# Kernel tuning notes

Measured on AMD Instinct MI355X. Metric: run time of the kernel, lower is better.

Reference implementation:

```python
import jax, jax.numpy as jnp
import numpy as np

HEADS = 4
DIM_HEAD = 64
SCALE = 8.0
EPS = 1e-5  # fp32 branch of the original LayerNorm


def setup_inputs() -> dict:
    key = jax.random.key(0)
    k1, k2, k3 = jax.random.split(key, 3)
    B, C, F, H, W = 2, 256, 4, 32, 32
    inner = HEADS * DIM_HEAD  # 256
    x = jax.random.normal(k1, (B, C, F, H, W), dtype=jnp.float32)
    gamma = jnp.ones((1, C, 1, 1, 1), dtype=jnp.float32)
    w_qkv = jax.random.normal(k2, (3 * inner, C), dtype=jnp.float32) * 0.05
    w_out = jax.random.normal(k3, (C, inner), dtype=jnp.float32) * 0.05
    return {"x": x, "gamma": gamma, "w_qkv": w_qkv, "w_out": w_out}


def _l2norm(t):
    return t / jnp.sqrt(jnp.sum(t * t, axis=-1, keepdims=True) + 1e-12)


def reference(x, gamma, w_qkv, w_out):
    B, C, F, H, W = x.shape
    N = F * H * W
    inner = HEADS * DIM_HEAD
    residual = x

    # channel LayerNorm (biased variance over dim=1)
    mean = jnp.mean(x, axis=1, keepdims=True)
    var = jnp.mean((x - mean) ** 2, axis=1, keepdims=True)
    xn = (x - mean) / jnp.sqrt(var + EPS) * gamma

    # 1x1x1 conv == channel matmul; flatten spatial dims to sequence
    xn_flat = xn.reshape(B, C, N)                      # [B, C, N]
    qkv = jnp.einsum('oc,bcn->bon', w_qkv, xn_flat)    # [B, 3*inner, N]
    qkv = qkv.reshape(B, 3, HEADS, DIM_HEAD, N)        # chunk then split heads
    qkv = jnp.transpose(qkv, (1, 0, 2, 4, 3))          # [3, B, h, N, d]
    q, k, v = qkv[0], qkv[1], qkv[2]

    q = _l2norm(q)
    k = _l2norm(k)

    sim = jnp.einsum('bhid,bhjd->bhij', q, k) * SCALE  # [B, h, N, N]
    attn = jax.nn.softmax(sim, axis=-1)
    out = jnp.einsum('bhij,bhjd->bhid', attn, v)       # [B, h, N, d]

    # 'b h n d -> b (h d) n' then 1x1x1 out conv
    out = jnp.transpose(out, (0, 1, 3, 2)).reshape(B, inner, N)
    out = jnp.einsum('oi,bin->bon', w_out, out).reshape(B, C, F, H, W)
    return out + residual
```

## Files before the change

### kernel.cpp

```cpp
#include <hip/hip_runtime.h>

#define BATCH 2
#define CCH   256
#define NSEQ  4096
#define NH    4
#define DH    64
#define INNER 256

typedef __attribute__((ext_vector_type(8))) __bf16 bf16x8;
typedef __attribute__((ext_vector_type(4))) float f32x4;
typedef __attribute__((ext_vector_type(8))) unsigned short u16x8;
typedef __attribute__((ext_vector_type(4))) unsigned short u16x4;
typedef __attribute__((ext_vector_type(4))) short s16x4;

#define GLD16(gsrc, ldst)                                                     \
  __builtin_amdgcn_global_load_lds(                                           \
      (const __attribute__((address_space(1))) unsigned int*)(const void*)(gsrc), \
      (__attribute__((address_space(3))) unsigned int*)(void*)(ldst), 16, 0, 0)

static __device__ __forceinline__ unsigned short f2bfr(float f) {
  union { float f; unsigned u; } v; v.f = f;
  return (unsigned short)((v.u + 0x8000u) >> 16);
}
static __device__ __forceinline__ unsigned pack2(float f0, float f1) {
  union { float f; unsigned u; } a, b; a.f = f0; b.f = f1;
  return __builtin_amdgcn_perm(b.u + 0x8000u, a.u + 0x8000u, 0x07060302u);
}
static __device__ __forceinline__ float bf2f(unsigned short u) {
  union { unsigned u; float f; } v; v.u = ((unsigned)u) << 16;
  return v.f;
}
static __device__ __forceinline__ bf16x8 ldb(const unsigned short* p) {
  return *(const bf16x8*)p;
}
static __device__ __forceinline__ f32x4 mm(bf16x8 a, bf16x8 b, f32x4 c) {
  return __builtin_amdgcn_mfma_f32_16x16x32_bf16(a, b, c, 0, 0, 0);
}
static __device__ __forceinline__ f32x4 mm16(s16x4 a, s16x4 b, f32x4 c) {
  return __builtin_amdgcn_mfma_f32_16x16x16bf16_1k(a, b, c, 0, 0, 0);
}

__global__ __launch_bounds__(256) void k_lncvt(const float* __restrict__ x,
                                               const float* __restrict__ gamma,
                                               unsigned short* __restrict__ xn,
                                               const float* __restrict__ wq,
                                               const float* __restrict__ wo,
                                               unsigned short* __restrict__ wqb,
                                               unsigned short* __restrict__ wob) {
  int blk = blockIdx.x;
  if (blk >= 256) {
    int t = (blk - 256) * 256 + threadIdx.x;
    int e = t * 4;
    if (e < 768 * 256) {
      float4 v = *(const float4*)(wq + e);
      u16x4 pk = { f2bfr(v.x), f2bfr(v.y), f2bfr(v.z), f2bfr(v.w) };
      *(u16x4*)(wqb + e) = pk;
    } else {
      int e2 = e - 768 * 256;
      float4 v = *(const float4*)(wo + e2);
      u16x4 pk = { f2bfr(v.x), f2bfr(v.y), f2bfr(v.z), f2bfr(v.w) };
      *(u16x4*)(wob + e2) = pk;
    }
    return;
  }
  int b  = blk >> 7;
  int n0 = (blk & 127) * 32;
  int t  = threadIdx.x;
  int nl = t & 31;
  int cg = t >> 5;
  int n  = n0 + nl;
  const float* xp = x + ((size_t)(b * CCH + cg * 32)) * NSEQ + n;
  float vals[32];
  float s = 0.f, s2 = 0.f;
#pragma unroll
  for (int j = 0; j < 32; j++) {
    float v = xp[(size_t)j * NSEQ];
    vals[j] = v; s += v; s2 += v * v;
  }
  __shared__ float rs[8][32], rs2[8][32];
  rs[cg][nl] = s; rs2[cg][nl] = s2;
  __syncthreads();
  float S = 0.f, S2 = 0.f;
#pragma unroll
  for (int g = 0; g < 8; g++) { S += rs[g][nl]; S2 += rs2[g][nl]; }
  float mean = S * (1.f / 256.f);
  float var  = S2 * (1.f / 256.f) - mean * mean;
  float rstd = rsqrtf(var + 1e-5f);
  unsigned short* dst = xn + ((size_t)b * NSEQ + n) * CCH + cg * 32;
#pragma unroll
  for (int j0 = 0; j0 < 32; j0 += 8) {
    u16x8 pk;
#pragma unroll
    for (int j = 0; j < 8; j++)
      pk[j] = f2bfr((vals[j0 + j] - mean) * rstd * gamma[cg * 32 + j0 + j]);
    *(u16x8*)(dst + j0) = pk;
  }
}

__global__ __launch_bounds__(256) void k_qkv(const unsigned short* __restrict__ wqb,
                                             const unsigned short* __restrict__ xn,
                                             unsigned short* __restrict__ vtb,
                                             unsigned short* __restrict__ qt,
                                             unsigned short* __restrict__ ktb) {
  int n0 = blockIdx.x * 64;
  int oi = blockIdx.y;
  int o0 = oi * 64;
  int b  = blockIdx.z;
  __shared__ unsigned short Al[64 * 128];
  __shared__ unsigned short Bl[64 * 128];
  int t = threadIdx.x;
  int lane = t & 63, w = t >> 6;
  int c = lane & 15, quad = lane >> 4;
  int wm = w >> 1, wn = w & 1;
  f32x4 acc[2][2] = {};
  int lr = lane >> 4;
  int lchk = lane & 15;
  const unsigned short* apg = wqb + (size_t)o0 * CCH;
  const unsigned short* bpg = xn + ((size_t)b * NSEQ + n0) * CCH;
  for (int kt = 0; kt < 2; kt++) {
    if (kt) __syncthreads();
#pragma unroll
    for (int q = 0; q < 4; q++) {
      int r = w * 16 + q * 4 + lr;
      int srcoff = r * CCH + kt * 128 + ((lchk ^ (r & 7)) * 8);
      GLD16(apg + srcoff, Al + (size_t)(w * 16 + q * 4) * 128);
      GLD16(bpg + srcoff, Bl + (size_t)(w * 16 + q * 4) * 128);
    }
    __syncthreads();
#pragma unroll
    for (int ks = 0; ks < 4; ks++) {
      int ra0 = wm * 32 + c, ra1 = ra0 + 16;
      int rb0 = wn * 32 + c, rb1 = rb0 + 16;
      bf16x8 a0 = ldb(&Al[ra0 * 128 + (((ks * 4 + quad) ^ (ra0 & 7)) * 8)]);
      bf16x8 a1 = ldb(&Al[ra1 * 128 + (((ks * 4 + quad) ^ (ra1 & 7)) * 8)]);
      bf16x8 b0 = ldb(&Bl[rb0 * 128 + (((ks * 4 + quad) ^ (rb0 & 7)) * 8)]);
      bf16x8 b1 = ldb(&Bl[rb1 * 128 + (((ks * 4 + quad) ^ (rb1 & 7)) * 8)]);
      acc[0][0] = mm(a0, b0, acc[0][0]);
      acc[0][1] = mm(a0, b1, acc[0][1]);
      acc[1][0] = mm(a1, b0, acc[1][0]);
      acc[1][1] = mm(a1, b1, acc[1][1]);
    }
  }
  if (oi < 8) {
    float* sq = (float*)Al;
    float s0 = 0.f, s1 = 0.f;
#pragma unroll
    for (int i = 0; i < 2; i++)
#pragma unroll
      for (int rr = 0; rr < 4; rr++) {
        s0 += acc[i][0][rr] * acc[i][0][rr];
        s1 += acc[i][1][rr] * acc[i][1][rr];
      }
    s0 += __shfl_xor(s0, 16); s0 += __shfl_xor(s0, 32);
    s1 += __shfl_xor(s1, 16); s1 += __shfl_xor(s1, 32);
    __syncthreads();
    if (quad == 0) {
      sq[wm * 64 + wn * 32 + c]      = s0;
      sq[wm * 64 + wn * 32 + 16 + c] = s1;
    }
    __syncthreads();
    float r0 = rsqrtf(sq[wn * 32 + c]      + sq[64 + wn * 32 + c]      + 1e-12f);
    float r1 = rsqrtf(sq[wn * 32 + 16 + c] + sq[64 + wn * 32 + 16 + c] + 1e-12f);
    if (oi < 4) { r0 *= 11.541560327111707f; r1 *= 11.541560327111707f; }
    int h = oi & 3;
    unsigned short* base = (oi < 4 ? qt : ktb) + ((size_t)(b * NH + h) * NSEQ) * DH;
#pragma unroll
    for (int i = 0; i < 2; i++)
#pragma unroll
      for (int j = 0; j < 2; j++) {
        float rsc = j ? r1 : r0;
        int n = n0 + wn * 32 + j * 16 + c;
        int d = wm * 32 + i * 16 + quad * 4;
        uint2 pk = { pack2(acc[i][j][0] * rsc, acc[i][j][1] * rsc),
                     pack2(acc[i][j][2] * rsc, acc[i][j][3] * rsc) };
        *(uint2*)(base + (size_t)n * DH + d) = pk;
      }
  } else {
    int h = oi - 8;
    unsigned short* vb = vtb + (size_t)(b * NH + h) * DH * NSEQ;
#pragma unroll
    for (int i = 0; i < 2; i++)
#pragma unroll
      for (int j = 0; j < 2; j++)
#pragma unroll
        for (int rr = 0; rr < 4; rr++) {
          int d = wm * 32 + i * 16 + quad * 4 + rr;
          int n = n0 + wn * 32 + j * 16 + c;
          vb[(size_t)d * NSEQ + n] = f2bfr(acc[i][j][rr]);
        }
  }
}

__global__ __launch_bounds__(256, 4) void k_attn(
    const unsigned short* __restrict__ qt,
    const unsigned short* __restrict__ ktb,
    const unsigned short* __restrict__ vtb,
    unsigned short* __restrict__ opart,
    float* __restrict__ lpart,
    int S, int kvlen) {
  int i0 = blockIdx.x * 128;
  int h  = blockIdx.y;
  int bz = blockIdx.z;
  int b  = bz / S, s = bz % S;
  __shared__ unsigned short Kl[64 * 64];
  __shared__ unsigned short Vl[64 * 64];
  int t = threadIdx.x;
  int lane = t & 63, w = t >> 6;
  int c = lane & 15, quad = lane >> 4;

  const unsigned short* qbase = qt  + ((size_t)(b * NH + h) * NSEQ) * DH;
  const unsigned short* kbase = ktb + ((size_t)(b * NH + h) * NSEQ) * DH;
  const unsigned short* vbase = vtb + (size_t)(b * NH + h) * DH * NSEQ;

  int rlo = w * 32 + c, rhi = rlo + 16;
  const unsigned short* qlo = qbase + (size_t)(i0 + rlo) * DH + quad * 8;
  const unsigned short* qhi = qlo + 16 * DH;
  bf16x8 qlo0 = ldb(qlo), qlo1 = ldb(qlo + 32);
  bf16x8 qhi0 = ldb(qhi), qhi1 = ldb(qhi + 32);

  s16x4 ones4;
#pragma unroll
  for (int j = 0; j < 4; j++) ones4[j] = (short)0x3F80;

  f32x4 acc[2][4] = {};
  f32x4 accl[2] = {};

  int slr = lane >> 3, slc = lane & 7;
  int ssw = (slc ^ slr) * 8;
  const unsigned short* kp = kbase + (size_t)(s * kvlen + w * 16 + slr) * DH + ssw;
  const unsigned short* vp = vbase + (size_t)(w * 16 + slr) * NSEQ + s * kvlen + ssw;
  int sw0 = (quad ^ (c & 7)) * 8;
  int sw1 = sw0 ^ 32;

  int nIt = kvlen / 64;
  for (int it = 0; it < nIt; it++) {
    if (it) __syncthreads();
    GLD16(kp,            &Kl[(w * 16)     * 64]);
    GLD16(kp + 8 * DH,   &Kl[(w * 16 + 8) * 64]);
    GLD16(vp,            &Vl[(w * 16)     * 64]);
    GLD16(vp + 8 * NSEQ, &Vl[(w * 16 + 8) * 64]);
    kp += 64 * DH; vp += 64;
    __syncthreads();

    s16x4 pf[2][4];
#pragma unroll
    for (int jt = 0; jt < 4; jt++) {
      bf16x8 k0 = ldb(&Kl[(jt * 16 + c) * 64 + sw0]);
      bf16x8 k1 = ldb(&Kl[(jt * 16 + c) * 64 + sw1]);
      f32x4 zl = {}; zl = mm(k0, qlo0, zl); zl = mm(k1, qlo1, zl);
      f32x4 zh = {}; zh = mm(k0, qhi0, zh); zh = mm(k1, qhi1, zh);
      uint2 pl = { pack2(exp2f(zl[0]), exp2f(zl[1])),
                   pack2(exp2f(zl[2]), exp2f(zl[3])) };
      pf[0][jt] = *(s16x4*)&pl;
      uint2 ph = { pack2(exp2f(zh[0]), exp2f(zh[1])),
                   pack2(exp2f(zh[2]), exp2f(zh[3])) };
      pf[1][jt] = *(s16x4*)&ph;
      accl[0] = mm16(ones4, pf[0][jt], accl[0]);
      accl[1] = mm16(ones4, pf[1][jt], accl[1]);
    }
#pragma unroll
    for (int dt = 0; dt < 4; dt++) {
      int row = dt * 16 + c;
      int rx = row & 7;
#pragma unroll
      for (int jt = 0; jt < 4; jt++) {
        int cj = jt * 2 + (quad >> 1);
        s16x4 a = *(const s16x4*)&Vl[row * 64 + (((cj ^ rx) * 8) | ((quad & 1) * 4))];
        acc[0][dt] = mm16(a, pf[0][jt], acc[0][dt]);
        acc[1][dt] = mm16(a, pf[1][jt], acc[1][dt]);
      }
    }
  }

  size_t rb = ((size_t)(b * NH + h) * S + s) * NSEQ + i0 + w * 32;
  if (quad == 0) {
    lpart[rb + c]      = accl[0][0];
    lpart[rb + 16 + c] = accl[1][0];
  }
#pragma unroll
  for (int dt = 0; dt < 4; dt++) {
    uint2 p0 = { pack2(acc[0][dt][0], acc[0][dt][1]),
                 pack2(acc[0][dt][2], acc[0][dt][3]) };
    *(uint2*)&opart[(rb + c) * 64 + dt * 16 + quad * 4] = p0;
    uint2 p1 = { pack2(acc[1][dt][0], acc[1][dt][1]),
                 pack2(acc[1][dt][2], acc[1][dt][3]) };
    *(uint2*)&opart[(rb + 16 + c) * 64 + dt * 16 + quad * 4] = p1;
  }
}

__global__ __launch_bounds__(256) void k_outm(
    const unsigned short* __restrict__ wob,
    const unsigned short* __restrict__ opart,
    const float* __restrict__ lpart,
    const float* __restrict__ x,
    float* __restrict__ out, int S) {
  int n0 = blockIdx.x * 32;
  int b  = blockIdx.y;
  __shared__ unsigned short Bl[32 * 256];
  int t = threadIdx.x;
  int lane = t & 63, w = t >> 6;
  int c = lane & 15, quad = lane >> 4;

  {
    int r = t >> 3, j = t & 7;
    int h = j >> 1, dl0 = (j & 1) * 32;
    float l = 0.f;
    for (int s = 0; s < S; s++)
      l += lpart[((size_t)(b * NH + h) * S + s) * NSEQ + n0 + r];
    float inv = 1.f / l;
    float o[32];
#pragma unroll
    for (int e = 0; e < 32; e++) o[e] = 0.f;
    for (int s = 0; s < S; s++) {
      const unsigned short* p =
          opart + (((size_t)(b * NH + h) * S + s) * NSEQ + n0 + r) * 64 + dl0;
      u16x8 v0 = *(const u16x8*)p;
      u16x8 v1 = *(const u16x8*)(p + 8);
      u16x8 v2 = *(const u16x8*)(p + 16);
      u16x8 v3 = *(const u16x8*)(p + 24);
#pragma unroll
      for (int e = 0; e < 8; e++) {
        o[e]      += bf2f(v0[e]);
        o[8 + e]  += bf2f(v1[e]);
        o[16 + e] += bf2f(v2[e]);
        o[24 + e] += bf2f(v3[e]);
      }
    }
#pragma unroll
    for (int cc = 0; cc < 4; cc++) {
      int cj = j * 4 + cc;
      uint4 pk = { pack2(o[cc*8+0]*inv, o[cc*8+1]*inv),
                   pack2(o[cc*8+2]*inv, o[cc*8+3]*inv),
                   pack2(o[cc*8+4]*inv, o[cc*8+5]*inv),
                   pack2(o[cc*8+6]*inv, o[cc*8+7]*inv) };
      *(uint4*)&Bl[r * 256 + ((cj ^ (r & 7)) * 8)] = pk;
    }
  }
  __syncthreads();

  f32x4 acc[4][2] = {};
  const unsigned short* ap = wob + (size_t)(w * 64) * INNER;
#pragma unroll
  for (int ks = 0; ks < 8; ks++) {
    bf16x8 b0 = ldb(&Bl[c * 256        + (((ks * 4 + quad) ^ (c & 7)) * 8)]);
    bf16x8 b1 = ldb(&Bl[(16 + c) * 256 + (((ks * 4 + quad) ^ (c & 7)) * 8)]);
#pragma unroll
    for (int ot = 0; ot < 4; ot++) {
      bf16x8 a = ldb(ap + (size_t)(ot * 16 + c) * INNER + ks * 32 + quad * 8);
      acc[ot][0] = mm(a, b0, acc[ot][0]);
      acc[ot][1] = mm(a, b1, acc[ot][1]);
    }
  }
#pragma unroll
  for (int ot = 0; ot < 4; ot++)
#pragma unroll
    for (int jn = 0; jn < 2; jn++)
#pragma unroll
      for (int rr = 0; rr < 4; rr++) {
        int o = w * 64 + ot * 16 + quad * 4 + rr;
        int n = n0 + jn * 16 + c;
        size_t idx = ((size_t)b * CCH + o) * NSEQ + n;
        out[idx] = acc[ot][jn][rr] + x[idx];
      }
}

extern "C" void kernel_launch(void* const* d_in, const int* in_sizes, int n_in,
                              void* d_out, int out_size, void* d_ws, size_t ws_size,
                              hipStream_t stream) {
  const float* x     = (const float*)d_in[0];
  const float* gamma = (const float*)d_in[1];
  const float* wq    = (const float*)d_in[2];
  const float* wo    = (const float*)d_in[3];
  float* out = (float*)d_out;

  const size_t MB = 1u << 20;
  char* ws = (char*)d_ws;
  unsigned short* xn  = (unsigned short*)ws;
  unsigned short* vtb = (unsigned short*)(ws + 4 * MB);
  unsigned short* wqb = (unsigned short*)(ws + 8 * MB);
  unsigned short* wob = (unsigned short*)(ws + 8 * MB + 512 * 1024);
  unsigned short* qt  = (unsigned short*)(ws + 9 * MB);
  unsigned short* ktb = (unsigned short*)(ws + 13 * MB);
  unsigned short* opart = (unsigned short*)(ws + 17 * MB);
  int S;
  if (ws_size >= 36 * MB) S = 4;
  else if (ws_size >= 27 * MB) S = 2;
  else S = 1;
  size_t opart_bytes = (size_t)S * BATCH * NH * NSEQ * DH * 2;
  float* lpart = (float*)(ws + 17 * MB + opart_bytes);
  int kvlen = NSEQ / S;

  k_lncvt<<<dim3(512),          256, 0, stream>>>(x, gamma, xn, wq, wo, wqb, wob);
  k_qkv  <<<dim3(64, 12, 2),    256, 0, stream>>>(wqb, xn, vtb, qt, ktb);
  k_attn <<<dim3(32, 4, 2 * S), 256, 0, stream>>>(qt, ktb, vtb, opart,
                                                  lpart, S, kvlen);
  k_outm <<<dim3(128, 2),       256, 0, stream>>>(wob, opart, lpart, x, out, S);
}
```

Measured before the change: 148.2 us.

## Double-buffer K/V tiles in attention and stage V transpose stores through LDS

The attention kernel now keeps two LDS buffers for K and V. It issues the asynchronous global-to-LDS loads for the next tile before computing on the current one, which replaces the two barriers per iteration with one and lets load latency overlap the MFMA work. Separately, the QKV projection kernel writes its transposed V output into shared memory first, then writes it to global memory as contiguous 16-byte vectors instead of scattered 2-byte stores. The trade-off is double the attention LDS footprint and an extra barrier pair in the projection epilogue. The overlap also depends on the compiler not inserting a conservative wait on all outstanding loads before the LDS reads.

```diff
diff --git a/kernel.cpp b/kernel.cpp
--- a/kernel.cpp
+++ b/kernel.cpp
@@ -177,7 +177,8 @@
       }
   } else {
     int h = oi - 8;
-    unsigned short* vb = vtb + (size_t)(b * NH + h) * DH * NSEQ;
+    __syncthreads();
+    unsigned short* st = Bl;
 #pragma unroll
     for (int i = 0; i < 2; i++)
 #pragma unroll
@@ -185,9 +186,16 @@
 #pragma unroll
         for (int rr = 0; rr < 4; rr++) {
           int d = wm * 32 + i * 16 + quad * 4 + rr;
-          int n = n0 + wn * 32 + j * 16 + c;
-          vb[(size_t)d * NSEQ + n] = f2bfr(acc[i][j][rr]);
+          int n = wn * 32 + j * 16 + c;
+          st[d * 72 + n] = f2bfr(acc[i][j][rr]);
         }
+    __syncthreads();
+    unsigned short* vb = vtb + (size_t)(b * NH + h) * DH * NSEQ;
+    int r = t >> 2, seg = (t & 3) * 16;
+    u16x8 w0 = *(const u16x8*)&st[r * 72 + seg];
+    u16x8 w1 = *(const u16x8*)&st[r * 72 + seg + 8];
+    *(u16x8*)(vb + (size_t)r * NSEQ + n0 + seg)     = w0;
+    *(u16x8*)(vb + (size_t)r * NSEQ + n0 + seg + 8) = w1;
   }
 }
 
@@ -202,8 +210,8 @@
   int h  = blockIdx.y;
   int bz = blockIdx.z;
   int b  = bz / S, s = bz % S;
-  __shared__ unsigned short Kl[64 * 64];
-  __shared__ unsigned short Vl[64 * 64];
+  __shared__ unsigned short Kl[2][64 * 64];
+  __shared__ unsigned short Vl[2][64 * 64];
   int t = threadIdx.x;
   int lane = t & 63, w = t >> 6;
   int c = lane & 15, quad = lane >> 4;
@@ -233,20 +241,29 @@
   int sw1 = sw0 ^ 32;
 
   int nIt = kvlen / 64;
+  GLD16(kp,            &Kl[0][(w * 16)     * 64]);
+  GLD16(kp + 8 * DH,   &Kl[0][(w * 16 + 8) * 64]);
+  GLD16(vp,            &Vl[0][(w * 16)     * 64]);
+  GLD16(vp + 8 * NSEQ, &Vl[0][(w * 16 + 8) * 64]);
+  kp += 64 * DH; vp += 64;
+
   for (int it = 0; it < nIt; it++) {
-    if (it) __syncthreads();
-    GLD16(kp,            &Kl[(w * 16)     * 64]);
-    GLD16(kp + 8 * DH,   &Kl[(w * 16 + 8) * 64]);
-    GLD16(vp,            &Vl[(w * 16)     * 64]);
-    GLD16(vp + 8 * NSEQ, &Vl[(w * 16 + 8) * 64]);
-    kp += 64 * DH; vp += 64;
-    __syncthreads();
+    int cur = it & 1;
+    __syncthreads();
+    if (it + 1 < nIt) {
+      int nb = cur ^ 1;
+      GLD16(kp,            &Kl[nb][(w * 16)     * 64]);
+      GLD16(kp + 8 * DH,   &Kl[nb][(w * 16 + 8) * 64]);
+      GLD16(vp,            &Vl[nb][(w * 16)     * 64]);
+      GLD16(vp + 8 * NSEQ, &Vl[nb][(w * 16 + 8) * 64]);
+      kp += 64 * DH; vp += 64;
+    }
 
     s16x4 pf[2][4];
 #pragma unroll
     for (int jt = 0; jt < 4; jt++) {
-      bf16x8 k0 = ldb(&Kl[(jt * 16 + c) * 64 + sw0]);
-      bf16x8 k1 = ldb(&Kl[(jt * 16 + c) * 64 + sw1]);
+      bf16x8 k0 = ldb(&Kl[cur][(jt * 16 + c) * 64 + sw0]);
+      bf16x8 k1 = ldb(&Kl[cur][(jt * 16 + c) * 64 + sw1]);
       f32x4 zl = {}; zl = mm(k0, qlo0, zl); zl = mm(k1, qlo1, zl);
       f32x4 zh = {}; zh = mm(k0, qhi0, zh); zh = mm(k1, qhi1, zh);
       uint2 pl = { pack2(exp2f(zl[0]), exp2f(zl[1])),
@@ -265,7 +282,7 @@
 #pragma unroll
       for (int jt = 0; jt < 4; jt++) {
         int cj = jt * 2 + (quad >> 1);
-        s16x4 a = *(const s16x4*)&Vl[row * 64 + (((cj ^ rx) * 8) | ((quad & 1) * 4))];
+        s16x4 a = *(const s16x4*)&Vl[cur][row * 64 + (((cj ^ rx) * 8) | ((quad & 1) * 4))];
         acc[0][dt] = mm16(a, pf[0][jt], acc[0][dt]);
         acc[1][dt] = mm16(a, pf[1][jt], acc[1][dt]);
       }
```

Result: no change. 150.7 us (+1.7%).

## Stage softmax probabilities through LDS to use 16x16x32 MFMA for PV

Applied to the files above, without the earlier changes.

The attention kernel now writes the exponentiated scores P to a swizzled LDS tile and reads them back as 8-wide bf16 fragments. This lets both the PV product and the row-sum use the 16x16x32 MFMA instead of twice as many 16x16x16 MFMAs, which halves the matrix instruction count for that stage. In exchange it adds 16KB of LDS per block plus extra LDS traffic, which can lower occupancy, and the outputs are now written as scalar bf16 stores. Separately, the output-projection kernel now handles 16 columns per block, doubling its grid size to spread the work across more blocks.

```diff
diff --git a/kernel.cpp b/kernel.cpp
--- a/kernel.cpp
+++ b/kernel.cpp
@@ -11,7 +11,6 @@
 typedef __attribute__((ext_vector_type(4))) float f32x4;
 typedef __attribute__((ext_vector_type(8))) unsigned short u16x8;
 typedef __attribute__((ext_vector_type(4))) unsigned short u16x4;
-typedef __attribute__((ext_vector_type(4))) short s16x4;
 
 #define GLD16(gsrc, ldst)                                                     \
   __builtin_amdgcn_global_load_lds(                                           \
@@ -35,9 +34,6 @@
 }
 static __device__ __forceinline__ f32x4 mm(bf16x8 a, bf16x8 b, f32x4 c) {
   return __builtin_amdgcn_mfma_f32_16x16x32_bf16(a, b, c, 0, 0, 0);
-}
-static __device__ __forceinline__ f32x4 mm16(s16x4 a, s16x4 b, f32x4 c) {
-  return __builtin_amdgcn_mfma_f32_16x16x16bf16_1k(a, b, c, 0, 0, 0);
 }
 
 __global__ __launch_bounds__(256) void k_lncvt(const float* __restrict__ x,
@@ -204,6 +200,7 @@
   int b  = bz / S, s = bz % S;
   __shared__ unsigned short Kl[64 * 64];
   __shared__ unsigned short Vl[64 * 64];
+  __shared__ unsigned short Pl[128 * 64];
   int t = threadIdx.x;
   int lane = t & 63, w = t >> 6;
   int c = lane & 15, quad = lane >> 4;
@@ -218,12 +215,13 @@
   bf16x8 qlo0 = ldb(qlo), qlo1 = ldb(qlo + 32);
   bf16x8 qhi0 = ldb(qhi), qhi1 = ldb(qhi + 32);
 
-  s16x4 ones4;
-#pragma unroll
-  for (int j = 0; j < 4; j++) ones4[j] = (short)0x3F80;
-
-  f32x4 acc[2][4] = {};
-  f32x4 accl[2] = {};
+  u16x8 onesu;
+#pragma unroll
+  for (int j = 0; j < 8; j++) onesu[j] = 0x3F80;
+  bf16x8 ones = *(bf16x8*)&onesu;
+
+  f32x4 acclo[4] = {}, acchi[4] = {};
+  f32x4 accllo = {}, acclhi = {};
 
   int slr = lane >> 3, slc = lane & 7;
   int ssw = (slc ^ slr) * 8;
@@ -231,6 +229,7 @@
   const unsigned short* vp = vbase + (size_t)(w * 16 + slr) * NSEQ + s * kvlen + ssw;
   int sw0 = (quad ^ (c & 7)) * 8;
   int sw1 = sw0 ^ 32;
+  int r7 = rlo & 7;
 
   int nIt = kvlen / 64;
   for (int it = 0; it < nIt; it++) {
@@ -242,50 +241,53 @@
     kp += 64 * DH; vp += 64;
     __syncthreads();
 
-    s16x4 pf[2][4];
 #pragma unroll
     for (int jt = 0; jt < 4; jt++) {
       bf16x8 k0 = ldb(&Kl[(jt * 16 + c) * 64 + sw0]);
       bf16x8 k1 = ldb(&Kl[(jt * 16 + c) * 64 + sw1]);
       f32x4 zl = {}; zl = mm(k0, qlo0, zl); zl = mm(k1, qlo1, zl);
       f32x4 zh = {}; zh = mm(k0, qhi0, zh); zh = mm(k1, qhi1, zh);
-      uint2 pl = { pack2(exp2f(zl[0]), exp2f(zl[1])),
-                   pack2(exp2f(zl[2]), exp2f(zl[3])) };
-      pf[0][jt] = *(s16x4*)&pl;
-      uint2 ph = { pack2(exp2f(zh[0]), exp2f(zh[1])),
-                   pack2(exp2f(zh[2]), exp2f(zh[3])) };
-      pf[1][jt] = *(s16x4*)&ph;
-      accl[0] = mm16(ones4, pf[0][jt], accl[0]);
-      accl[1] = mm16(ones4, pf[1][jt], accl[1]);
-    }
+      int cj = jt * 2 + (quad >> 1);
+      int sub = (quad & 1) * 4;
+      uint2 pkl = { pack2(exp2f(zl[0]), exp2f(zl[1])),
+                    pack2(exp2f(zl[2]), exp2f(zl[3])) };
+      *(uint2*)&Pl[rlo * 64 + ((cj ^ r7) * 8) + sub] = pkl;
+      uint2 pkh = { pack2(exp2f(zh[0]), exp2f(zh[1])),
+                    pack2(exp2f(zh[2]), exp2f(zh[3])) };
+      *(uint2*)&Pl[rhi * 64 + ((cj ^ r7) * 8) + sub] = pkh;
+    }
+    bf16x8 plo0 = ldb(&Pl[rlo * 64 + ((quad ^ r7) * 8)]);
+    bf16x8 plo1 = ldb(&Pl[rlo * 64 + (((quad + 4) ^ r7) * 8)]);
+    bf16x8 phi0 = ldb(&Pl[rhi * 64 + ((quad ^ r7) * 8)]);
+    bf16x8 phi1 = ldb(&Pl[rhi * 64 + (((quad + 4) ^ r7) * 8)]);
 #pragma unroll
     for (int dt = 0; dt < 4; dt++) {
-      int row = dt * 16 + c;
-      int rx = row & 7;
-#pragma unroll
-      for (int jt = 0; jt < 4; jt++) {
-        int cj = jt * 2 + (quad >> 1);
-        s16x4 a = *(const s16x4*)&Vl[row * 64 + (((cj ^ rx) * 8) | ((quad & 1) * 4))];
-        acc[0][dt] = mm16(a, pf[0][jt], acc[0][dt]);
-        acc[1][dt] = mm16(a, pf[1][jt], acc[1][dt]);
-      }
-    }
+      bf16x8 v0 = ldb(&Vl[(dt * 16 + c) * 64 + sw0]);
+      bf16x8 v1 = ldb(&Vl[(dt * 16 + c) * 64 + sw1]);
+      acclo[dt] = mm(plo0, v0, acclo[dt]);
+      acclo[dt] = mm(plo1, v1, acclo[dt]);
+      acchi[dt] = mm(phi0, v0, acchi[dt]);
+      acchi[dt] = mm(phi1, v1, acchi[dt]);
+    }
+    accllo = mm(plo0, ones, accllo); accllo = mm(plo1, ones, accllo);
+    acclhi = mm(phi0, ones, acclhi); acclhi = mm(phi1, ones, acclhi);
   }
 
   size_t rb = ((size_t)(b * NH + h) * S + s) * NSEQ + i0 + w * 32;
-  if (quad == 0) {
-    lpart[rb + c]      = accl[0][0];
-    lpart[rb + 16 + c] = accl[1][0];
-  }
-#pragma unroll
-  for (int dt = 0; dt < 4; dt++) {
-    uint2 p0 = { pack2(acc[0][dt][0], acc[0][dt][1]),
-                 pack2(acc[0][dt][2], acc[0][dt][3]) };
-    *(uint2*)&opart[(rb + c) * 64 + dt * 16 + quad * 4] = p0;
-    uint2 p1 = { pack2(acc[1][dt][0], acc[1][dt][1]),
-                 pack2(acc[1][dt][2], acc[1][dt][3]) };
-    *(uint2*)&opart[(rb + 16 + c) * 64 + dt * 16 + quad * 4] = p1;
-  }
+  if (c == 0) {
+#pragma unroll
+    for (int rr = 0; rr < 4; rr++) {
+      lpart[rb + quad * 4 + rr]      = accllo[rr];
+      lpart[rb + 16 + quad * 4 + rr] = acclhi[rr];
+    }
+  }
+#pragma unroll
+  for (int rr = 0; rr < 4; rr++)
+#pragma unroll
+    for (int dt = 0; dt < 4; dt++) {
+      opart[(rb + quad * 4 + rr) * 64 + dt * 16 + c]      = f2bfr(acclo[dt][rr]);
+      opart[(rb + 16 + quad * 4 + rr) * 64 + dt * 16 + c] = f2bfr(acchi[dt][rr]);
+    }
 }
 
 __global__ __launch_bounds__(256) void k_outm(
@@ -294,41 +296,37 @@
     const float* __restrict__ lpart,
     const float* __restrict__ x,
     float* __restrict__ out, int S) {
-  int n0 = blockIdx.x * 32;
+  int n0 = blockIdx.x * 16;
   int b  = blockIdx.y;
-  __shared__ unsigned short Bl[32 * 256];
+  __shared__ unsigned short Bl[16 * 256];
   int t = threadIdx.x;
   int lane = t & 63, w = t >> 6;
   int c = lane & 15, quad = lane >> 4;
 
   {
-    int r = t >> 3, j = t & 7;
-    int h = j >> 1, dl0 = (j & 1) * 32;
+    int r = t >> 4, j = t & 15;
+    int h = j >> 2, dl0 = (j & 3) * 16;
     float l = 0.f;
     for (int s = 0; s < S; s++)
       l += lpart[((size_t)(b * NH + h) * S + s) * NSEQ + n0 + r];
     float inv = 1.f / l;
-    float o[32];
-#pragma unroll
-    for (int e = 0; e < 32; e++) o[e] = 0.f;
+    float o[16];
+#pragma unroll
+    for (int e = 0; e < 16; e++) o[e] = 0.f;
     for (int s = 0; s < S; s++) {
       const unsigned short* p =
           opart + (((size_t)(b * NH + h) * S + s) * NSEQ + n0 + r) * 64 + dl0;
       u16x8 v0 = *(const u16x8*)p;
       u16x8 v1 = *(const u16x8*)(p + 8);
-      u16x8 v2 = *(const u16x8*)(p + 16);
-      u16x8 v3 = *(const u16x8*)(p + 24);
 #pragma unroll
       for (int e = 0; e < 8; e++) {
-        o[e]      += bf2f(v0[e]);
-        o[8 + e]  += bf2f(v1[e]);
-        o[16 + e] += bf2f(v2[e]);
-        o[24 + e] += bf2f(v3[e]);
+        o[e]     += bf2f(v0[e]);
+        o[8 + e] += bf2f(v1[e]);
       }
     }
 #pragma unroll
-    for (int cc = 0; cc < 4; cc++) {
-      int cj = j * 4 + cc;
+    for (int cc = 0; cc < 2; cc++) {
+      int cj = j * 2 + cc;
       uint4 pk = { pack2(o[cc*8+0]*inv, o[cc*8+1]*inv),
                    pack2(o[cc*8+2]*inv, o[cc*8+3]*inv),
                    pack2(o[cc*8+4]*inv, o[cc*8+5]*inv),
@@ -338,30 +336,26 @@
   }
   __syncthreads();
 
-  f32x4 acc[4][2] = {};
+  f32x4 acc[4] = {};
   const unsigned short* ap = wob + (size_t)(w * 64) * INNER;
 #pragma unroll
   for (int ks = 0; ks < 8; ks++) {
-    bf16x8 b0 = ldb(&Bl[c * 256        + (((ks * 4 + quad) ^ (c & 7)) * 8)]);
-    bf16x8 b1 = ldb(&Bl[(16 + c) * 256 + (((ks * 4 + quad) ^ (c & 7)) * 8)]);
+    bf16x8 b0 = ldb(&Bl[c * 256 + (((ks * 4 + quad) ^ (c & 7)) * 8)]);
 #pragma unroll
     for (int ot = 0; ot < 4; ot++) {
       bf16x8 a = ldb(ap + (size_t)(ot * 16 + c) * INNER + ks * 32 + quad * 8);
-      acc[ot][0] = mm(a, b0, acc[ot][0]);
-      acc[ot][1] = mm(a, b1, acc[ot][1]);
+      acc[ot] = mm(a, b0, acc[ot]);
     }
   }
 #pragma unroll
   for (int ot = 0; ot < 4; ot++)
 #pragma unroll
-    for (int jn = 0; jn < 2; jn++)
-#pragma unroll
-      for (int rr = 0; rr < 4; rr++) {
-        int o = w * 64 + ot * 16 + quad * 4 + rr;
-        int n = n0 + jn * 16 + c;
-        size_t idx = ((size_t)b * CCH + o) * NSEQ + n;
-        out[idx] = acc[ot][jn][rr] + x[idx];
-      }
+    for (int rr = 0; rr < 4; rr++) {
+      int o = w * 64 + ot * 16 + quad * 4 + rr;
+      int n = n0 + c;
+      size_t idx = ((size_t)b * CCH + o) * NSEQ + n;
+      out[idx] = acc[ot][rr] + x[idx];
+    }
 }
 
 extern "C" void kernel_launch(void* const* d_in, const int* in_sizes, int n_in,
@@ -394,5 +388,5 @@
   k_qkv  <<<dim3(64, 12, 2),    256, 0, stream>>>(wqb, xn, vtb, qt, ktb);
   k_attn <<<dim3(32, 4, 2 * S), 256, 0, stream>>>(qt, ktb, vtb, opart,
                                                   lpart, S, kvlen);
-  k_outm <<<dim3(128, 2),       256, 0, stream>>>(wob, opart, lpart, x, out, S);
-}
+  k_outm <<<dim3(256, 2),       256, 0, stream>>>(wob, opart, lpart, x, out, S);
+}
```

Measured after the change: 150.5 us. About the same (+1.6%).
